# Optimization experiments

Measured on AMD Instinct MI355X. Metric: run time of the kernel, lower is better.

The kernel has to match this reference:

```python
import jax, jax.numpy as jnp
import numpy as np

B, L, H, T = 32, 512, 768, 8  # batch, tokens, dim_hidden, num_trees
DK = H // T


def setup_inputs() -> dict:
    key = jax.random.key(0)
    ks = jax.random.split(key, 8)
    s = 1.0 / np.sqrt(H)
    return {
        "input": jax.random.normal(ks[0], (B, L, H), dtype=jnp.float32),
        "src_mask": jax.random.randint(ks[1], (B, L), 0, 2, dtype=jnp.int32),
        "Wq": jax.random.uniform(ks[2], (H, H), minval=-s, maxval=s, dtype=jnp.float32),
        "bq": jax.random.uniform(ks[3], (H,), minval=-s, maxval=s, dtype=jnp.float32),
        "Wk": jax.random.uniform(ks[4], (H, H), minval=-s, maxval=s, dtype=jnp.float32),
        "bk": jax.random.uniform(ks[5], (H,), minval=-s, maxval=s, dtype=jnp.float32),
        "Wroot": jax.random.uniform(ks[6], (T, H), minval=-s, maxval=s, dtype=jnp.float32),
        "broot": jax.random.uniform(ks[7], (T,), minval=-s, maxval=s, dtype=jnp.float32),
    }


def reference(input, src_mask, Wq, bq, Wk, bk, Wroot, broot):
    x = input
    # multi-head attention probabilities (eval mode, no dropout)
    q = (x @ Wq.T + bq).reshape(B, L, T, DK).transpose(0, 2, 1, 3)  # (B,T,L,DK)
    k = (x @ Wk.T + bk).reshape(B, L, T, DK).transpose(0, 2, 1, 3)
    scores = jnp.einsum("btqd,btkd->btqk", q, k) / jnp.sqrt(jnp.float32(DK))
    scores = jnp.where(src_mask[:, None, None, :] == 0, -1e9, scores)
    p_attn = jax.nn.softmax(scores, axis=-1)  # (B,T,L,L) == f_ij per tree

    # root scores f_i per tree: (B,T,L)
    f = jnp.einsum("blh,th->btl", x, Wroot) + broot[None, :, None]

    eye = jnp.eye(L, dtype=x.dtype)
    A = jnp.exp(p_attn) * (1.0 - eye)           # zero diagonal
    deg = A.sum(axis=2)                          # column sums (dim=1 per tree)
    Lap = -A + deg[..., None, :] * eye           # Laplacian, deg on diagonal
    Lbar = Lap.at[:, :, 0, :].set(f)             # replace first row with root scores

    LLinv = jnp.linalg.inv(Lbar)                 # (B,T,L,L)
    d0 = f * LLinv[..., 0]                       # f_i * LLinv[:, :, 0]  -> (B,T,L)
    diag = jnp.diagonal(LLinv, axis1=-2, axis2=-1)  # (B,T,L)
    tmp1 = A * diag[..., None, :]                # A[i,j] * LLinv[j,j]
    tmp2 = A * jnp.swapaxes(LLinv, -1, -2)       # A[i,j] * LLinv[j,i]
    col_mask = (jnp.arange(L) != 0).astype(x.dtype)[None, None, None, :]  # zero first col
    row_mask = (jnp.arange(L) != 0).astype(x.dtype)[None, None, :, None]  # zero first row
    dx = col_mask * tmp1 - row_mask * tmp2       # (B,T,L,L)

    d = jnp.concatenate([d0[..., None, :], dx], axis=-2)  # (B,T,L+1,L)
    df = jnp.swapaxes(d, -1, -2)                 # (B,T,L,L+1)
    att = df[..., 1:]                            # (B,T,L,L); stacked adj_list
    return att
```

## Files before the change

### kernel.cpp

```cpp
#include <hip/hip_runtime.h>
#include <math.h>

#define NB_ 64
#define NPH 8

__global__ __launch_bounds__(256) void proj_gemm(const float* __restrict__ x,
    const float* __restrict__ Wq, const float* __restrict__ bq,
    const float* __restrict__ Wk, const float* __restrict__ bk,
    float* __restrict__ Qb, float* __restrict__ Kb) {
  const float* W    = blockIdx.z ? Wk : Wq;
  const float* bias = blockIdx.z ? bk : bq;
  float* out        = blockIdx.z ? Kb : Qb;
  const int m0 = blockIdx.x * 128;
  const int n0 = blockIdx.y * 128;
  __shared__ float Xs[16][132];
  __shared__ float Ws2[16][132];
  const int tid = threadIdx.x;
  const int tm = tid & 15, tn = tid >> 4;
  float acc[8][8];
#pragma unroll
  for (int i = 0; i < 8; i++)
#pragma unroll
    for (int j = 0; j < 8; j++) acc[i][j] = 0.f;

  for (int kk = 0; kk < 768; kk += 16) {
#pragma unroll
    for (int rep = 0; rep < 2; rep++) {
      int fidx = tid + rep * 256;
      int row = fidx >> 2, f4i = fidx & 3;
      float4 v = ((const float4*)(x + (size_t)(m0 + row) * 768 + kk))[f4i];
      Xs[f4i * 4 + 0][row] = v.x; Xs[f4i * 4 + 1][row] = v.y;
      Xs[f4i * 4 + 2][row] = v.z; Xs[f4i * 4 + 3][row] = v.w;
    }
#pragma unroll
    for (int rep = 0; rep < 2; rep++) {
      int fidx = tid + rep * 256;
      int row = fidx >> 2, f4i = fidx & 3;
      float4 v = ((const float4*)(W + (size_t)(n0 + row) * 768 + kk))[f4i];
      Ws2[f4i * 4 + 0][row] = v.x; Ws2[f4i * 4 + 1][row] = v.y;
      Ws2[f4i * 4 + 2][row] = v.z; Ws2[f4i * 4 + 3][row] = v.w;
    }
    __syncthreads();
#pragma unroll
    for (int k = 0; k < 16; k++) {
      float4 a0 = *(const float4*)&Xs[k][tm * 4];
      float4 a1 = *(const float4*)&Xs[k][tm * 4 + 64];
      float4 b0 = *(const float4*)&Ws2[k][tn * 4];
      float4 b1 = *(const float4*)&Ws2[k][tn * 4 + 64];
      float am[8] = {a0.x,a0.y,a0.z,a0.w,a1.x,a1.y,a1.z,a1.w};
      float bn[8] = {b0.x,b0.y,b0.z,b0.w,b1.x,b1.y,b1.z,b1.w};
#pragma unroll
      for (int i = 0; i < 8; i++)
#pragma unroll
        for (int j = 0; j < 8; j++) acc[i][j] += am[i] * bn[j];
    }
    __syncthreads();
  }
  float bA[4], bB[4];
#pragma unroll
  for (int j = 0; j < 4; j++) {
    bA[j] = bias[n0 + tn * 4 + j];
    bB[j] = bias[n0 + 64 + tn * 4 + j];
  }
#pragma unroll
  for (int half = 0; half < 2; half++)
#pragma unroll
    for (int i = 0; i < 4; i++) {
      const int row = m0 + half * 64 + tm * 4 + i;
      float4 oA = {acc[half*4+i][0] + bA[0], acc[half*4+i][1] + bA[1],
                   acc[half*4+i][2] + bA[2], acc[half*4+i][3] + bA[3]};
      *(float4*)(out + (size_t)row * 768 + n0 + tn * 4) = oA;
      float4 oB = {acc[half*4+i][4] + bB[0], acc[half*4+i][5] + bB[1],
                   acc[half*4+i][6] + bB[2], acc[half*4+i][7] + bB[3]};
      *(float4*)(out + (size_t)row * 768 + n0 + 64 + tn * 4) = oB;
    }
}

__global__ __launch_bounds__(256) void f_kernel(const float* __restrict__ x,
    const float* __restrict__ Wroot, const float* __restrict__ broot,
    float* __restrict__ fout) {
  int row = blockIdx.x * 256 + threadIdx.x;
  int b = row >> 9, l = row & 511;
  float acc[8] = {0,0,0,0,0,0,0,0};
  const float4* xr = (const float4*)(x + (size_t)row * 768);
  for (int h4 = 0; h4 < 192; h4++) {
    float4 xv = xr[h4];
#pragma unroll
    for (int t = 0; t < 8; t++) {
      float4 wv = ((const float4*)(Wroot + (size_t)t * 768))[h4];
      acc[t] += xv.x * wv.x + xv.y * wv.y + xv.z * wv.z + xv.w * wv.w;
    }
  }
#pragma unroll
  for (int t = 0; t < 8; t++)
    fout[(size_t)((b * 8 + t) << 9) + l] = acc[t] + broot[t];
}

__global__ __launch_bounds__(256) void scores_kernel(const float* __restrict__ Qb,
    const float* __restrict__ Kb, const int* __restrict__ mask,
    float* __restrict__ A) {
  const int lin = blockIdx.x;
  const int xcd = lin & 7;
  const int idx = lin >> 3;
  const int bt  = xcd * 32 + (idx >> 5);
  const int q0  = (idx & 31) * 16;
  const int b = bt >> 3, t = bt & 7;
  __shared__ float  S[16][512];
  __shared__ float4 Qs4[16][24];
  __shared__ float  part[16][16];
  __shared__ float  invsum[16];
  const int tid = threadIdx.x;
  for (int i = tid; i < 384; i += 256) {
    int q = i / 24, f4 = i % 24;
    Qs4[q][f4] =
        ((const float4*)(Qb + (size_t)(b * 512 + q0 + q) * 768 + t * 96))[f4];
  }
  __syncthreads();
  const float scl = 0.10206207261596575f;
#pragma unroll 1
  for (int rep = 0; rep < 2; rep++) {
    const int k = rep * 256 + tid;
    const float4* kr = (const float4*)(Kb + (size_t)(b * 512 + k) * 768 + t * 96);
    float acc[16];
#pragma unroll
    for (int q = 0; q < 16; q++) acc[q] = 0.f;
#pragma unroll 4
    for (int f4 = 0; f4 < 24; f4++) {
      float4 kv = kr[f4];
#pragma unroll
      for (int q = 0; q < 16; q++) {
        float4 qv = Qs4[q][f4];
        acc[q] += qv.x * kv.x + qv.y * kv.y + qv.z * kv.z + qv.w * kv.w;
      }
    }
    int mk = mask[b * 512 + k];
#pragma unroll
    for (int q = 0; q < 16; q++)
      S[q][k] = mk ? expf(acc[q] * scl) : 0.f;
  }
  __syncthreads();
  { int q = tid >> 4, j = tid & 15;
    float s = 0.f;
#pragma unroll
    for (int i = 0; i < 32; i++) s += S[q][j + 16 * i];
    part[q][j] = s; }
  __syncthreads();
  if (tid < 16) {
    float s = 0.f;
#pragma unroll
    for (int j = 0; j < 16; j++) s += part[tid][j];
    invsum[tid] = 1.f / fmaxf(s, 1e-30f);
  }
  __syncthreads();
#pragma unroll 1
  for (int rep = 0; rep < 2; rep++) {
    const int k = rep * 256 + tid;
#pragma unroll
    for (int q = 0; q < 16; q++) {
      float p = S[q][k] * invsum[q];
      float a = (q0 + q == k) ? 0.f : expf(p);
      A[(size_t)(bt * 512 + q0 + q) * 512 + k] = a;
    }
  }
}

__global__ __launch_bounds__(256) void build_kernel(const float* __restrict__ A,
    const float* __restrict__ fin, float* __restrict__ M) {
  const int bt = blockIdx.y;
  const int k = blockIdx.x * 256 + threadIdx.x;
  const float* Ab = A + (size_t)bt * 262144;
  float* Mb = M + (size_t)bt * 262144;
  float s = 0.f;
  { float a = Ab[k]; s += a; Mb[k] = fin[bt * 512 + k]; }
  for (int q = 1; q < 512; q++) {
    float a = Ab[(size_t)q * 512 + k];
    s += a;
    Mb[(size_t)q * 512 + k] = -a;
  }
  if (k != 0) Mb[(size_t)k * 512 + k] = s;
}

__global__ __launch_bounds__(512) void panel_kernel(float* __restrict__ M,
    int* __restrict__ pivr, float* __restrict__ Stg, int* __restrict__ rowslot,
    int ph) {
  const int bt = blockIdx.x, tid = threadIdx.x;
  const int j0 = ph * NB_;
  __shared__ float rowj[NB_];
  __shared__ float bufj[NB_], bufr[NB_];
  __shared__ float pivval_s;
  __shared__ unsigned long long wred[8];
  __shared__ int pivlist[NB_];
  __shared__ int perm_s[512];
  __shared__ int srcrow[128];
  __shared__ int cnt;
  float* Mb = M + (size_t)bt * 262144;
  float r[NB_];
  {
    const float4* p0 = (const float4*)(Mb + (size_t)tid * 512 + j0);
#pragma unroll
    for (int fi = 0; fi < 16; fi++) {
      float4 a = p0[fi];
      r[4*fi] = a.x; r[4*fi+1] = a.y; r[4*fi+2] = a.z; r[4*fi+3] = a.w;
    }
  }
  const int lane = tid & 63, wv = tid >> 6;
  for (int l = 0; l < NB_; l++) {
    const int j = j0 + l;
    float v = 0.f;
#pragma unroll
    for (int c = 0; c < NB_; c++) v = (c == l) ? r[c] : v;
    float best = -1.f; int bidx = 0;
    if (tid >= j) { best = fabsf(v); bidx = tid; }
    unsigned long long pk = (best >= 0.f)
        ? ((((unsigned long long)__float_as_uint(best)) << 32) | (unsigned)bidx) : 0ull;
#pragma unroll
    for (int off = 32; off > 0; off >>= 1) {
      unsigned long long o = __shfl_xor(pk, off, 64);
      if (o > pk) pk = o;
    }
    if (lane == 0) wred[wv] = pk;
    __syncthreads();
    unsigned long long ma = wred[0];
#pragma unroll
    for (int w = 1; w < 8; w++) ma = (wred[w] > ma) ? wred[w] : ma;
    const int rr = (int)(unsigned)(ma & 0xffffffffull);
    if (tid == rr) {
      pivval_s = v;
#pragma unroll
      for (int c = 0; c < NB_; c++) bufr[c] = r[c];
    }
    if (tid == j) {
#pragma unroll
      for (int c = 0; c < NB_; c++) bufj[c] = r[c];
    }
    if (tid == 0) pivlist[l] = rr;
    __syncthreads();
    const float rinv = 1.f / pivval_s;
    if (tid == j) {
#pragma unroll
      for (int c = 0; c < NB_; c++) {
        float nv = (c == l) ? rinv : bufr[c] * rinv;
        r[c] = nv;
        rowj[c] = nv;
      }
    }
    if (rr != j && tid == rr) {
#pragma unroll
      for (int c = 0; c < NB_; c++) r[c] = bufj[c];
    }
    __syncthreads();
    if (tid != j) {
      float m = 0.f;
#pragma unroll
      for (int c = 0; c < NB_; c++) m = (c == l) ? r[c] : m;
#pragma unroll
      for (int c = 0; c < NB_; c++) r[c] = ((c == l) ? 0.f : r[c]) - m * rowj[c];
    }
    __syncthreads();
  }
  {
    float4* p0 = (float4*)(Mb + (size_t)tid * 512 + j0);
#pragma unroll
    for (int fi = 0; fi < 16; fi++) {
      float4 a = {r[4*fi], r[4*fi+1], r[4*fi+2], r[4*fi+3]};
      p0[fi] = a;
    }
  }
  if (tid < NB_) pivr[bt * 512 + j0 + tid] = pivlist[tid];

  if (tid < 512) perm_s[tid] = tid;
  if (tid == 0) cnt = 0;
  __syncthreads();
  if (tid == 0) {
    for (int l = 0; l < NB_; l++) {
      int rw = pivlist[l];
      int tp = perm_s[j0 + l]; perm_s[j0 + l] = perm_s[rw]; perm_s[rw] = tp;
    }
  }
  __syncthreads();
  {
    int s = -1;
    if (perm_s[tid] != tid) { s = atomicAdd(&cnt, 1); srcrow[s] = perm_s[tid]; }
    rowslot[bt * 512 + tid] = s;
  }
  __syncthreads();
  const int nmv = cnt;
  float* Sb = Stg + (size_t)bt * 98304;
  for (int idx = tid; idx < 64 * 128; idx += 512) {
    int l = idx >> 7, f4 = idx & 127;
    ((float4*)(Sb + (size_t)l * 512))[f4] =
        ((const float4*)(Mb + (size_t)perm_s[j0 + l] * 512))[f4];
  }
  for (int idx = tid; idx < nmv * 128; idx += 512) {
    int s = idx >> 7, f4 = idx & 127;
    ((float4*)(Sb + (size_t)(64 + s) * 512))[f4] =
        ((const float4*)(Mb + (size_t)srcrow[s] * 512))[f4];
  }
}

__global__ __launch_bounds__(256) void update_kernel(float* __restrict__ M,
    const float* __restrict__ Stg, const int* __restrict__ rowslot, int ph) {
  const int lin = blockIdx.x;
  const int xcd = lin & 7;
  const int idx = lin >> 3;
  const int bt  = xcd * 32 + (idx / 28);
  const int tl  = idx % 28;
  const int rt  = tl / 7;
  int ct = tl % 7;
  ct += (ct >= ph) ? 1 : 0;
  const int i0 = rt * 128, c0 = ct * 64;
  const int j0 = ph * NB_;
  float* Mb = M + (size_t)bt * 262144;
  const float* Sb = Stg + (size_t)bt * 98304;
  __shared__ float Vs[16][132];
  __shared__ float Xs[16][68];
  __shared__ int rs_s[128];
  const int tid = threadIdx.x;
  const int tm = tid & 15, tn = tid >> 4;
  if (tid < 128) rs_s[tid] = rowslot[bt * 512 + i0 + tid];
  float acc[8][4];
#pragma unroll
  for (int i = 0; i < 8; i++)
#pragma unroll
    for (int j = 0; j < 4; j++) acc[i][j] = 0.f;

#pragma unroll 1
  for (int kk = 0; kk < 64; kk += 16) {
#pragma unroll
    for (int rep = 0; rep < 2; rep++) {
      int fidx = tid + rep * 256;
      int row = fidx >> 2, f4i = fidx & 3;
      float4 v = *(const float4*)(Mb + (size_t)(i0 + row) * 512 + j0 + kk + f4i * 4);
      Vs[f4i * 4 + 0][row] = v.x; Vs[f4i * 4 + 1][row] = v.y;
      Vs[f4i * 4 + 2][row] = v.z; Vs[f4i * 4 + 3][row] = v.w;
    }
    {
      int row = tid >> 4, f4i = tid & 15;
      float4 v = *(const float4*)(Sb + (size_t)(kk + row) * 512 + c0 + f4i * 4);
      *(float4*)&Xs[row][f4i * 4] = v;
    }
    __syncthreads();
#pragma unroll
    for (int k = 0; k < 16; k++) {
      float4 a0 = *(const float4*)&Vs[k][tm * 4];
      float4 a1 = *(const float4*)&Vs[k][tm * 4 + 64];
      float4 bv = *(const float4*)&Xs[k][tn * 4];
      float am[8] = {a0.x,a0.y,a0.z,a0.w,a1.x,a1.y,a1.z,a1.w};
      float bn[4] = {bv.x,bv.y,bv.z,bv.w};
#pragma unroll
      for (int i = 0; i < 8; i++)
#pragma unroll
        for (int j = 0; j < 4; j++) acc[i][j] += am[i] * bn[j];
    }
    __syncthreads();
  }
  const int colg = c0 + tn * 4;
#pragma unroll
  for (int half = 0; half < 2; half++)
#pragma unroll
    for (int i = 0; i < 4; i++) {
      const int rl = half * 64 + tm * 4 + i;
      const int row = i0 + rl;
      const int rs = rs_s[rl];
      const float* oldp = (rs >= 0) ? (Sb + (size_t)(64 + rs) * 512 + colg)
                                    : (Mb + (size_t)row * 512 + colg);
      float4 o = *(const float4*)oldp;
      o.x += acc[half*4+i][0]; o.y += acc[half*4+i][1];
      o.z += acc[half*4+i][2]; o.w += acc[half*4+i][3];
      if (row >= j0 && row < j0 + NB_) {
        float4 xr = *(const float4*)(Sb + (size_t)(row - j0) * 512 + colg);
        o.x -= xr.x; o.y -= xr.y; o.z -= xr.z; o.w -= xr.w;
      }
      *(float4*)(Mb + (size_t)row * 512 + colg) = o;
    }
}

__global__ __launch_bounds__(64) void colsrc_kernel(const int* __restrict__ pivr,
                                                    int* __restrict__ colsrc) {
  const int bt = blockIdx.x, tid = threadIdx.x;
  __shared__ int piv[512];
  __shared__ int cs[512];
  for (int i = tid; i < 512; i += 64) { piv[i] = pivr[bt * 512 + i]; cs[i] = i; }
  __syncthreads();
  if (tid == 0) {
    for (int j = 511; j >= 0; j--) { int r = piv[j]; int tp = cs[j]; cs[j] = cs[r]; cs[r] = tp; }
  }
  __syncthreads();
  for (int i = tid; i < 512; i += 64) colsrc[bt * 512 + i] = cs[i];
}

__global__ __launch_bounds__(256) void permute_kernel(float* __restrict__ M,
    const int* __restrict__ colsrc, float* __restrict__ diagv) {
  const int bt = blockIdx.y, r0 = blockIdx.x * 32;
  __shared__ int cs[512];
  __shared__ float rowbuf[4][512];
  const int tid = threadIdx.x;
  const int lane = tid & 63, w = tid >> 6;
  for (int i = tid; i < 512; i += 256) cs[i] = colsrc[bt * 512 + i];
  __syncthreads();
  float* Mb = M + (size_t)bt * 262144;
  for (int it = 0; it < 8; it++) {
    const int row = r0 + it * 4 + w;
    float4 v0 = ((const float4*)(Mb + (size_t)row * 512))[lane];
    float4 v1 = ((const float4*)(Mb + (size_t)row * 512))[lane + 64];
    *(float4*)&rowbuf[w][lane * 4] = v0;
    *(float4*)&rowbuf[w][256 + lane * 4] = v1;
    __syncthreads();
    float o[8];
#pragma unroll
    for (int j = 0; j < 8; j++) o[j] = rowbuf[w][cs[lane * 8 + j]];
    if ((row >> 3) == lane) {
#pragma unroll
      for (int j = 0; j < 8; j++)
        if ((row & 7) == j) diagv[bt * 512 + row] = o[j];
    }
    float4 oA = {o[0], o[1], o[2], o[3]};
    float4 oB = {o[4], o[5], o[6], o[7]};
    *(float4*)(Mb + (size_t)row * 512 + lane * 8) = oA;
    *(float4*)(Mb + (size_t)row * 512 + lane * 8 + 4) = oB;
    __syncthreads();
  }
}

__global__ __launch_bounds__(256) void final_kernel(const float* __restrict__ M,
    const float* __restrict__ diagv, float* __restrict__ Aout) {
  const int bt = blockIdx.y;
  int x = blockIdx.x, ti = 0;
  while (x >= 8 - ti) { x -= 8 - ti; ti++; }
  const int tj = ti + x;
  const int tid = threadIdx.x, c = tid & 63, g = tid >> 6;
  __shared__ float Aa[64][65];
  __shared__ float Ab[64][65];
  __shared__ float dgi[64], dgj[64];
  const size_t base = (size_t)bt * 262144;
  const float* Mb = M + base;
  float* Ao = Aout + base;
  if (tid < 64)       dgi[tid] = diagv[bt * 512 + ti * 64 + tid];
  else if (tid < 128) dgj[tid - 64] = diagv[bt * 512 + tj * 64 + (tid - 64)];
  for (int rr = g; rr < 64; rr += 4)
    Aa[rr][c] = Ao[(size_t)(tj * 64 + rr) * 512 + ti * 64 + c];
  if (ti != tj)
    for (int rr = g; rr < 64; rr += 4)
      Ab[rr][c] = Ao[(size_t)(ti * 64 + rr) * 512 + tj * 64 + c];
  __syncthreads();
  for (int kk = g; kk < 64; kk += 4) {
    int krow = ti * 64 + kk, q = tj * 64 + c;
    float a = Aa[c][kk];
    float llv = Mb[(size_t)krow * 512 + q];
    float val = 0.f;
    if (krow != 0) val = a * dgi[kk];
    if (q != 0)    val -= a * llv;
    Ao[(size_t)krow * 512 + q] = val;
  }
  if (ti != tj) {
    for (int kk = g; kk < 64; kk += 4) {
      int krow = tj * 64 + kk, q = ti * 64 + c;
      float a = Ab[c][kk];
      float llv = Mb[(size_t)krow * 512 + q];
      float val = 0.f;
      if (krow != 0) val = a * dgj[kk];
      if (q != 0)    val -= a * llv;
      Ao[(size_t)krow * 512 + q] = val;
    }
  }
}

extern "C" void kernel_launch(void* const* d_in, const int* in_sizes, int n_in,
                              void* d_out, int out_size, void* d_ws, size_t ws_size,
                              hipStream_t stream) {
  const float* x     = (const float*)d_in[0];
  const int*   mask  = (const int*)d_in[1];
  const float* Wq    = (const float*)d_in[2];
  const float* bq    = (const float*)d_in[3];
  const float* Wk    = (const float*)d_in[4];
  const float* bk    = (const float*)d_in[5];
  const float* Wroot = (const float*)d_in[6];
  const float* broot = (const float*)d_in[7];
  float* A = (float*)d_out;

  float* ws = (float*)d_ws;
  size_t off = 0;
  float* M    = ws + off; off += (size_t)256 * 512 * 512;
  float* Qb   = ws + off; off += (size_t)16384 * 768;
  float* Kb   = ws + off; off += (size_t)16384 * 768;
  float* fbuf = ws + off; off += (size_t)256 * 512;
  float* dgv  = ws + off; off += (size_t)256 * 512;
  int* pivr   = (int*)(ws + off); off += (size_t)256 * 512;
  int* csrc   = (int*)(ws + off); off += (size_t)256 * 512;
  int* rslot  = (int*)(ws + off); off += (size_t)256 * 512;
  if (ws_size < off * sizeof(float)) return;

  float* Stg = Qb;

  proj_gemm<<<dim3(128, 6, 2), 256, 0, stream>>>(x, Wq, bq, Wk, bk, Qb, Kb);
  f_kernel<<<64, 256, 0, stream>>>(x, Wroot, broot, fbuf);
  scores_kernel<<<dim3(8192), 256, 0, stream>>>(Qb, Kb, mask, A);
  build_kernel<<<dim3(2, 256), 256, 0, stream>>>(A, fbuf, M);
  for (int ph = 0; ph < NPH; ph++) {
    panel_kernel<<<256, 512, 0, stream>>>(M, pivr, Stg, rslot, ph);
    update_kernel<<<dim3(7168), 256, 0, stream>>>(M, Stg, rslot, ph);
  }
  colsrc_kernel<<<256, 64, 0, stream>>>(pivr, csrc);
  permute_kernel<<<dim3(16, 256), 256, 0, stream>>>(M, csrc, dgv);
  final_kernel<<<dim3(36, 256), 256, 0, stream>>>(M, dgv, A);
}
```

Measured before the change: 4.478 ms.

## Fuse Laplacian build into scores kernel and double LU panel width

Writes -A into the Laplacian matrix and accumulates column degrees with atomics inside the scores kernel, so the separate build pass that re-read all of A is replaced by a small diagonal/first-row fixup kernel. The blocked LU panel width goes from 64 to 128, halving the number of panel/update phases and kernel launches. The staging buffer now holds only the non-panel columns (384 wide) with fixed slots for the panel rows. The wider panel keeps 128 floats per thread in registers, which risks spills and low occupancy, and the atomics add contention on the degree buffer.

```diff
diff --git a/kernel.cpp b/kernel.cpp
--- a/kernel.cpp
+++ b/kernel.cpp
@@ -1,8 +1,8 @@
 #include <hip/hip_runtime.h>
 #include <math.h>
 
-#define NB_ 64
-#define NPH 8
+#define NB_ 128
+#define NPH 4
 
 __global__ __launch_bounds__(256) void proj_gemm(const float* __restrict__ x,
     const float* __restrict__ Wq, const float* __restrict__ bq,
@@ -78,8 +78,11 @@
 
 __global__ __launch_bounds__(256) void f_kernel(const float* __restrict__ x,
     const float* __restrict__ Wroot, const float* __restrict__ broot,
-    float* __restrict__ fout) {
+    float* __restrict__ fout, float* __restrict__ deg) {
   int row = blockIdx.x * 256 + threadIdx.x;
+  { float4 z = {0,0,0,0};
+    ((float4*)deg)[row * 2] = z;
+    ((float4*)deg)[row * 2 + 1] = z; }
   int b = row >> 9, l = row & 511;
   float acc[8] = {0,0,0,0,0,0,0,0};
   const float4* xr = (const float4*)(x + (size_t)row * 768);
@@ -98,7 +101,7 @@
 
 __global__ __launch_bounds__(256) void scores_kernel(const float* __restrict__ Qb,
     const float* __restrict__ Kb, const int* __restrict__ mask,
-    float* __restrict__ A) {
+    float* __restrict__ A, float* __restrict__ M, float* __restrict__ deg) {
   const int lin = blockIdx.x;
   const int xcd = lin & 7;
   const int idx = lin >> 3;
@@ -155,32 +158,28 @@
 #pragma unroll 1
   for (int rep = 0; rep < 2; rep++) {
     const int k = rep * 256 + tid;
+    float psum = 0.f;
 #pragma unroll
     for (int q = 0; q < 16; q++) {
       float p = S[q][k] * invsum[q];
       float a = (q0 + q == k) ? 0.f : expf(p);
       A[(size_t)(bt * 512 + q0 + q) * 512 + k] = a;
-    }
-  }
-}
-
-__global__ __launch_bounds__(256) void build_kernel(const float* __restrict__ A,
-    const float* __restrict__ fin, float* __restrict__ M) {
-  const int bt = blockIdx.y;
-  const int k = blockIdx.x * 256 + threadIdx.x;
-  const float* Ab = A + (size_t)bt * 262144;
+      M[(size_t)(bt * 512 + q0 + q) * 512 + k] = -a;
+      psum += a;
+    }
+    atomicAdd(&deg[bt * 512 + k], psum);
+  }
+}
+
+__global__ __launch_bounds__(512) void fixup_kernel(const float* __restrict__ fin,
+    const float* __restrict__ deg, float* __restrict__ M) {
+  const int bt = blockIdx.x, k = threadIdx.x;
   float* Mb = M + (size_t)bt * 262144;
-  float s = 0.f;
-  { float a = Ab[k]; s += a; Mb[k] = fin[bt * 512 + k]; }
-  for (int q = 1; q < 512; q++) {
-    float a = Ab[(size_t)q * 512 + k];
-    s += a;
-    Mb[(size_t)q * 512 + k] = -a;
-  }
-  if (k != 0) Mb[(size_t)k * 512 + k] = s;
-}
-
-__global__ __launch_bounds__(512) void panel_kernel(float* __restrict__ M,
+  if (k != 0) Mb[(size_t)k * 512 + k] = deg[bt * 512 + k];
+  Mb[k] = fin[bt * 512 + k];
+}
+
+__global__ __launch_bounds__(512, 2) void panel_kernel(float* __restrict__ M,
     int* __restrict__ pivr, float* __restrict__ Stg, int* __restrict__ rowslot,
     int ph) {
   const int bt = blockIdx.x, tid = threadIdx.x;
@@ -191,14 +190,14 @@
   __shared__ unsigned long long wred[8];
   __shared__ int pivlist[NB_];
   __shared__ int perm_s[512];
-  __shared__ int srcrow[128];
+  __shared__ int slotsrc[256];
   __shared__ int cnt;
   float* Mb = M + (size_t)bt * 262144;
   float r[NB_];
   {
     const float4* p0 = (const float4*)(Mb + (size_t)tid * 512 + j0);
 #pragma unroll
-    for (int fi = 0; fi < 16; fi++) {
+    for (int fi = 0; fi < 32; fi++) {
       float4 a = p0[fi];
       r[4*fi] = a.x; r[4*fi+1] = a.y; r[4*fi+2] = a.z; r[4*fi+3] = a.w;
     }
@@ -250,9 +249,7 @@
     }
     __syncthreads();
     if (tid != j) {
-      float m = 0.f;
-#pragma unroll
-      for (int c = 0; c < NB_; c++) m = (c == l) ? r[c] : m;
+      const float m = (tid == rr && rr != j) ? bufj[l] : v;
 #pragma unroll
       for (int c = 0; c < NB_; c++) r[c] = ((c == l) ? 0.f : r[c]) - m * rowj[c];
     }
@@ -261,14 +258,14 @@
   {
     float4* p0 = (float4*)(Mb + (size_t)tid * 512 + j0);
 #pragma unroll
-    for (int fi = 0; fi < 16; fi++) {
+    for (int fi = 0; fi < 32; fi++) {
       float4 a = {r[4*fi], r[4*fi+1], r[4*fi+2], r[4*fi+3]};
       p0[fi] = a;
     }
   }
   if (tid < NB_) pivr[bt * 512 + j0 + tid] = pivlist[tid];
 
-  if (tid < 512) perm_s[tid] = tid;
+  perm_s[tid] = tid;
   if (tid == 0) cnt = 0;
   __syncthreads();
   if (tid == 0) {
@@ -280,21 +277,19 @@
   __syncthreads();
   {
     int s = -1;
-    if (perm_s[tid] != tid) { s = atomicAdd(&cnt, 1); srcrow[s] = perm_s[tid]; }
+    if (tid >= j0 && tid < j0 + NB_) { s = tid - j0; slotsrc[s] = perm_s[tid]; }
+    else if (perm_s[tid] != tid)     { s = NB_ + atomicAdd(&cnt, 1); slotsrc[s] = perm_s[tid]; }
     rowslot[bt * 512 + tid] = s;
   }
   __syncthreads();
-  const int nmv = cnt;
-  float* Sb = Stg + (size_t)bt * 98304;
-  for (int idx = tid; idx < 64 * 128; idx += 512) {
-    int l = idx >> 7, f4 = idx & 127;
-    ((float4*)(Sb + (size_t)l * 512))[f4] =
-        ((const float4*)(Mb + (size_t)perm_s[j0 + l] * 512))[f4];
-  }
-  for (int idx = tid; idx < nmv * 128; idx += 512) {
-    int s = idx >> 7, f4 = idx & 127;
-    ((float4*)(Sb + (size_t)(64 + s) * 512))[f4] =
-        ((const float4*)(Mb + (size_t)srcrow[s] * 512))[f4];
+  const int ns = NB_ + cnt;
+  float* Sg = Stg + (size_t)bt * 98304;
+  const int jf4 = j0 >> 2;
+  for (int idxi = tid; idxi < ns * 96; idxi += 512) {
+    int s2 = idxi / 96, f4s = idxi % 96;
+    int gf4 = (f4s < jf4) ? f4s : f4s + 32;
+    ((float4*)(Sg + (size_t)s2 * 384))[f4s] =
+        ((const float4*)(Mb + (size_t)slotsrc[s2] * 512))[gf4];
   }
 }
 
@@ -303,15 +298,16 @@
   const int lin = blockIdx.x;
   const int xcd = lin & 7;
   const int idx = lin >> 3;
-  const int bt  = xcd * 32 + (idx / 28);
-  const int tl  = idx % 28;
-  const int rt  = tl / 7;
-  int ct = tl % 7;
-  ct += (ct >= ph) ? 1 : 0;
+  const int bt  = xcd * 32 + (idx / 24);
+  const int tl  = idx % 24;
+  const int rt  = tl / 6;
+  int ct = tl % 6;
+  ct += (ct >= ph * 2) ? 2 : 0;
   const int i0 = rt * 128, c0 = ct * 64;
   const int j0 = ph * NB_;
+  const int sc0 = (c0 < j0) ? c0 : c0 - NB_;
   float* Mb = M + (size_t)bt * 262144;
-  const float* Sb = Stg + (size_t)bt * 98304;
+  const float* Sg = Stg + (size_t)bt * 98304;
   __shared__ float Vs[16][132];
   __shared__ float Xs[16][68];
   __shared__ int rs_s[128];
@@ -325,7 +321,7 @@
     for (int j = 0; j < 4; j++) acc[i][j] = 0.f;
 
 #pragma unroll 1
-  for (int kk = 0; kk < 64; kk += 16) {
+  for (int kk = 0; kk < NB_; kk += 16) {
 #pragma unroll
     for (int rep = 0; rep < 2; rep++) {
       int fidx = tid + rep * 256;
@@ -336,7 +332,7 @@
     }
     {
       int row = tid >> 4, f4i = tid & 15;
-      float4 v = *(const float4*)(Sb + (size_t)(kk + row) * 512 + c0 + f4i * 4);
+      float4 v = *(const float4*)(Sg + (size_t)(kk + row) * 384 + sc0 + f4i * 4);
       *(float4*)&Xs[row][f4i * 4] = v;
     }
     __syncthreads();
@@ -354,7 +350,8 @@
     }
     __syncthreads();
   }
-  const int colg = c0 + tn * 4;
+  const int colg  = c0 + tn * 4;
+  const int scolg = sc0 + tn * 4;
 #pragma unroll
   for (int half = 0; half < 2; half++)
 #pragma unroll
@@ -362,13 +359,13 @@
       const int rl = half * 64 + tm * 4 + i;
       const int row = i0 + rl;
       const int rs = rs_s[rl];
-      const float* oldp = (rs >= 0) ? (Sb + (size_t)(64 + rs) * 512 + colg)
+      const float* oldp = (rs >= 0) ? (Sg + (size_t)rs * 384 + scolg)
                                     : (Mb + (size_t)row * 512 + colg);
       float4 o = *(const float4*)oldp;
       o.x += acc[half*4+i][0]; o.y += acc[half*4+i][1];
       o.z += acc[half*4+i][2]; o.w += acc[half*4+i][3];
       if (row >= j0 && row < j0 + NB_) {
-        float4 xr = *(const float4*)(Sb + (size_t)(row - j0) * 512 + colg);
+        float4 xr = *(const float4*)(Sg + (size_t)(row - j0) * 384 + scolg);
         o.x -= xr.x; o.y -= xr.y; o.z -= xr.z; o.w -= xr.w;
       }
       *(float4*)(Mb + (size_t)row * 512 + colg) = o;
@@ -484,6 +481,7 @@
   float* Qb   = ws + off; off += (size_t)16384 * 768;
   float* Kb   = ws + off; off += (size_t)16384 * 768;
   float* fbuf = ws + off; off += (size_t)256 * 512;
+  float* deg  = ws + off; off += (size_t)256 * 512;
   float* dgv  = ws + off; off += (size_t)256 * 512;
   int* pivr   = (int*)(ws + off); off += (size_t)256 * 512;
   int* csrc   = (int*)(ws + off); off += (size_t)256 * 512;
@@ -493,12 +491,12 @@
   float* Stg = Qb;
 
   proj_gemm<<<dim3(128, 6, 2), 256, 0, stream>>>(x, Wq, bq, Wk, bk, Qb, Kb);
-  f_kernel<<<64, 256, 0, stream>>>(x, Wroot, broot, fbuf);
-  scores_kernel<<<dim3(8192), 256, 0, stream>>>(Qb, Kb, mask, A);
-  build_kernel<<<dim3(2, 256), 256, 0, stream>>>(A, fbuf, M);
+  f_kernel<<<64, 256, 0, stream>>>(x, Wroot, broot, fbuf, deg);
+  scores_kernel<<<dim3(8192), 256, 0, stream>>>(Qb, Kb, mask, A, M, deg);
+  fixup_kernel<<<256, 512, 0, stream>>>(fbuf, deg, M);
   for (int ph = 0; ph < NPH; ph++) {
     panel_kernel<<<256, 512, 0, stream>>>(M, pivr, Stg, rslot, ph);
-    update_kernel<<<dim3(7168), 256, 0, stream>>>(M, Stg, rslot, ph);
+    update_kernel<<<dim3(6144), 256, 0, stream>>>(M, Stg, rslot, ph);
   }
   colsrc_kernel<<<256, 64, 0, stream>>>(pivr, csrc);
   permute_kernel<<<dim3(16, 256), 256, 0, stream>>>(M, csrc, dgv);
```

Result: slower. 5.297 ms (+18.3%).
